# Kernel tuning notes

Measured on AMD Instinct MI355X. Metric: run time of the kernel, lower is better.

Reference implementation:

```python
import jax, jax.numpy as jnp
import numpy as np


def setup_inputs() -> dict:
    key = jax.random.key(0)
    k1, k2 = jax.random.split(key)
    B, S, N, D = 4, 8, 2048, 3
    pred_points = jax.random.normal(k1, (B, S, N, D), dtype=jnp.float32)
    target_points = jax.random.normal(k2, (B, S, N, D), dtype=jnp.float32)
    return {"pred_points": pred_points, "target_points": target_points}


def reference(pred_points, target_points):
    # pred_points, target_points: [B, S, N, 3]
    seq_len = pred_points.shape[1]
    # Pairwise Euclidean distances via the GEMM identity |p-t|^2 = |p|^2 + |t|^2 - 2 p.t
    p2 = jnp.sum(pred_points * pred_points, axis=-1)      # [B,S,N]
    t2 = jnp.sum(target_points * target_points, axis=-1)  # [B,S,M]
    cross = jnp.einsum('bsnd,bsmd->bsnm', pred_points, target_points)  # [B,S,N,M]
    d2 = p2[..., :, None] + t2[..., None, :] - 2.0 * cross
    d = jnp.sqrt(jnp.maximum(d2, 0.0))  # [B,S,N,M]
    # Bidirectional nearest-neighbor min + mean over points
    min_p2t = jnp.min(d, axis=3)  # [B,S,N]
    min_t2p = jnp.min(d, axis=2)  # [B,S,M]
    chamfer = jnp.mean(min_p2t, axis=2) + jnp.mean(min_t2p, axis=2)  # [B,S]
    total_loss = jnp.sum(chamfer, axis=1)  # [B] (sum over timesteps)
    # reduction == 'mean'
    return jnp.mean(total_loss) / seq_len
```

## Files before the change

kernel.cpp:

```cpp
#include <hip/hip_runtime.h>
#include <math.h>

#define N_PTS   2048
#define BLOCK   256
#define NQ      8
#define SLAB    128
#define NSLAB   (N_PTS / SLAB)

__global__ __launch_bounds__(BLOCK) void chamfer_min_kernel(
    const float* __restrict__ pred,
    const float* __restrict__ tgt,
    unsigned int* __restrict__ wsmin)
{
    __shared__ float4 sh[SLAB];

    const int bs   = blockIdx.x;
    const int dir  = blockIdx.y;
    const int slab = blockIdx.z;
    const int tid  = threadIdx.x;

    const float* Abase = (dir ? tgt : pred) + (size_t)bs * N_PTS * 3;
    const float* Bbase = (dir ? pred : tgt) + (size_t)bs * N_PTS * 3;

    if (tid < SLAB) {
        const int j = slab * SLAB + tid;
        const float x = Bbase[3 * j + 0];
        const float y = Bbase[3 * j + 1];
        const float z = Bbase[3 * j + 2];
        sh[tid] = make_float4(x, y, z, x * x + y * y + z * z);
    }
    __syncthreads();

    float nx[NQ], ny[NQ], nz[NQ], p2[NQ], best[NQ];
    #pragma unroll
    for (int k = 0; k < NQ; ++k) {
        const int q = tid + BLOCK * k;
        const float px = Abase[3 * q + 0];
        const float py = Abase[3 * q + 1];
        const float pz = Abase[3 * q + 2];
        nx[k] = -2.0f * px;
        ny[k] = -2.0f * py;
        nz[k] = -2.0f * pz;
        p2[k] = px * px + py * py + pz * pz;
        best[k] = 3.4e38f;
    }

    #pragma unroll 2
    for (int j = 0; j < SLAB; ++j) {
        const float4 t = sh[j];
        #pragma unroll
        for (int k = 0; k < NQ; ++k) {
            const float v = fmaf(nx[k], t.x,
                            fmaf(ny[k], t.y,
                            fmaf(nz[k], t.z, t.w)));
            best[k] = fminf(best[k], v);
        }
    }

    const int base = (dir * 32 + bs) * N_PTS;
    #pragma unroll
    for (int k = 0; k < NQ; ++k) {
        const float d2 = fmaxf(p2[k] + best[k], 0.0f);
        atomicMin(&wsmin[base + tid + BLOCK * k], __float_as_uint(d2));
    }
}

__global__ __launch_bounds__(BLOCK) void chamfer_finalize_kernel(
    const float4* __restrict__ wsmin,
    float* __restrict__ out)
{
    __shared__ float red[BLOCK / 64];
    const int i = blockIdx.x * BLOCK + threadIdx.x;
    const float4 t = wsmin[i];
    float s = sqrtf(t.x) + sqrtf(t.y) + sqrtf(t.z) + sqrtf(t.w);

    for (int off = 32; off > 0; off >>= 1)
        s += __shfl_down(s, off, 64);
    const int tid = threadIdx.x;
    if ((tid & 63) == 0) red[tid >> 6] = s;
    __syncthreads();
    if (tid == 0) {
        const float blk = red[0] + red[1] + red[2] + red[3];
        atomicAdd(out, blk * (1.0f / 65536.0f));
    }
}

extern "C" void kernel_launch(void* const* d_in, const int* in_sizes, int n_in,
                              void* d_out, int out_size, void* d_ws, size_t ws_size,
                              hipStream_t stream) {
    const float* pred = (const float*)d_in[0];
    const float* tgt  = (const float*)d_in[1];
    float* out = (float*)d_out;
    unsigned int* wsmin = (unsigned int*)d_ws;

    hipMemsetAsync(wsmin, 0x7F, (size_t)131072 * sizeof(unsigned int), stream);
    hipMemsetAsync(out, 0, sizeof(float), stream);

    dim3 grid(32, 2, NSLAB);
    chamfer_min_kernel<<<grid, BLOCK, 0, stream>>>(pred, tgt, wsmin);

    chamfer_finalize_kernel<<<131072 / (BLOCK * 4), BLOCK, 0, stream>>>(
        (const float4*)wsmin, out);
}
```

Baseline: 81.03 us.

## Replace atomicMin partials with per-slab buffers reduced in finalize kernel

Each min block now writes its per-slab partial squared distances to a dedicated workspace slot, so the global atomicMin and the 0x7F memset of the workspace go away. The finalize kernel takes the min across the 16 slabs per point before the sqrt and the sum. The inner loop also processes two target points per iteration to raise ILP. The cost is a larger workspace (64 × 16 × 2048 floats) and extra global traffic in finalize; the launch count drops by one memset.

```diff
diff --git a/kernel.cpp b/kernel.cpp
--- a/kernel.cpp
+++ b/kernel.cpp
@@ -10,7 +10,7 @@
 __global__ __launch_bounds__(BLOCK) void chamfer_min_kernel(
     const float* __restrict__ pred,
     const float* __restrict__ tgt,
-    unsigned int* __restrict__ wsmin)
+    float* __restrict__ part)
 {
     __shared__ float4 sh[SLAB];
 
@@ -45,39 +45,49 @@
         best[k] = 3.4e38f;
     }
 
-    #pragma unroll 2
-    for (int j = 0; j < SLAB; ++j) {
-        const float4 t = sh[j];
+    #pragma unroll 4
+    for (int j = 0; j < SLAB; j += 2) {
+        const float4 t0 = sh[j];
+        const float4 t1 = sh[j + 1];
         #pragma unroll
         for (int k = 0; k < NQ; ++k) {
-            const float v = fmaf(nx[k], t.x,
-                            fmaf(ny[k], t.y,
-                            fmaf(nz[k], t.z, t.w)));
-            best[k] = fminf(best[k], v);
+            const float v0 = fmaf(nx[k], t0.x,
+                             fmaf(ny[k], t0.y,
+                             fmaf(nz[k], t0.z, t0.w)));
+            const float v1 = fmaf(nx[k], t1.x,
+                             fmaf(ny[k], t1.y,
+                             fmaf(nz[k], t1.z, t1.w)));
+            best[k] = fminf(fminf(best[k], v0), v1);
         }
     }
 
-    const int base = (dir * 32 + bs) * N_PTS;
+    float* dst = part + ((size_t)((dir * 32 + bs) * NSLAB + slab)) * N_PTS;
     #pragma unroll
-    for (int k = 0; k < NQ; ++k) {
-        const float d2 = fmaxf(p2[k] + best[k], 0.0f);
-        atomicMin(&wsmin[base + tid + BLOCK * k], __float_as_uint(d2));
-    }
+    for (int k = 0; k < NQ; ++k)
+        dst[tid + BLOCK * k] = p2[k] + best[k];
 }
 
 __global__ __launch_bounds__(BLOCK) void chamfer_finalize_kernel(
-    const float4* __restrict__ wsmin,
+    const float* __restrict__ part,
     float* __restrict__ out)
 {
     __shared__ float red[BLOCK / 64];
-    const int i = blockIdx.x * BLOCK + threadIdx.x;
-    const float4 t = wsmin[i];
-    float s = sqrtf(t.x) + sqrtf(t.y) + sqrtf(t.z) + sqrtf(t.w);
+    const int g     = blockIdx.x * BLOCK + threadIdx.x;
+    const int dirbs = g >> 11;
+    const int q     = g & (N_PTS - 1);
+    const float* src = part + ((size_t)dirbs * NSLAB) * N_PTS + q;
+
+    float m = src[0];
+    #pragma unroll
+    for (int s = 1; s < NSLAB; ++s)
+        m = fminf(m, src[(size_t)s * N_PTS]);
+
+    float d = sqrtf(fmaxf(m, 0.0f));
 
     for (int off = 32; off > 0; off >>= 1)
-        s += __shfl_down(s, off, 64);
+        d += __shfl_down(d, off, 64);
     const int tid = threadIdx.x;
-    if ((tid & 63) == 0) red[tid >> 6] = s;
+    if ((tid & 63) == 0) red[tid >> 6] = d;
     __syncthreads();
     if (tid == 0) {
         const float blk = red[0] + red[1] + red[2] + red[3];
@@ -91,14 +101,12 @@
     const float* pred = (const float*)d_in[0];
     const float* tgt  = (const float*)d_in[1];
     float* out = (float*)d_out;
-    unsigned int* wsmin = (unsigned int*)d_ws;
+    float* part = (float*)d_ws;
 
-    hipMemsetAsync(wsmin, 0x7F, (size_t)131072 * sizeof(unsigned int), stream);
     hipMemsetAsync(out, 0, sizeof(float), stream);
 
     dim3 grid(32, 2, NSLAB);
-    chamfer_min_kernel<<<grid, BLOCK, 0, stream>>>(pred, tgt, wsmin);
+    chamfer_min_kernel<<<grid, BLOCK, 0, stream>>>(pred, tgt, part);
 
-    chamfer_finalize_kernel<<<131072 / (BLOCK * 4), BLOCK, 0, stream>>>(
-        (const float4*)wsmin, out);
+    chamfer_finalize_kernel<<<(64 * N_PTS) / BLOCK, BLOCK, 0, stream>>>(part, out);
 }
```

Measured after the change: 88.41 us. 1.09x slower.
